# Kernel optimization log

Hardware: AMD Instinct MI355X
Metric: run time of the kernel (lower is better)

The kernel has to match this reference:

```python
import jax, jax.numpy as jnp
import numpy as np

B, L, D, N = 2, 2048, 1024, 16
DT_MIN, DT_MAX = 1e-3, 1e-1


def setup_inputs() -> dict:
    key = jax.random.key(0)
    ks = jax.random.split(key, 8)
    u = jax.random.normal(ks[0], (B, L, D), dtype=jnp.float32)
    # torch.nn.Linear weights are (out_features, in_features)
    W_dt = jax.random.normal(ks[1], (D, D), dtype=jnp.float32) * 0.02
    b_dt = jnp.zeros((D,), dtype=jnp.float32)
    W_B = jax.random.normal(ks[2], (D * N, D), dtype=jnp.float32) * 0.02
    b_B = jnp.zeros((D * N,), dtype=jnp.float32)
    W_C = jax.random.normal(ks[3], (D * N, D), dtype=jnp.float32) * 0.02
    b_C = jnp.zeros((D * N,), dtype=jnp.float32)
    # log_A init: log(1..N) broadcast over channels (HiPPO-ish diagonal)
    log_A = jnp.broadcast_to(jnp.log(jnp.arange(1, N + 1, dtype=jnp.float32)), (D, N))
    D_skip = jnp.ones((D,), dtype=jnp.float32)
    lo, hi = float(np.log(DT_MIN)), float(np.log(DT_MAX))
    dt_bias = jax.random.uniform(ks[4], (D,), dtype=jnp.float32) * (hi - lo) + lo
    return {"u": u, "log_A": log_A, "D_skip": D_skip, "dt_bias": dt_bias,
            "W_dt": W_dt, "b_dt": b_dt, "W_B": W_B, "b_B": b_B,
            "W_C": W_C, "b_C": b_C}


def reference(u, log_A, D_skip, dt_bias, W_dt, b_dt, W_B, b_B, W_C, b_C):
    b, l, d = u.shape
    n = log_A.shape[1]
    A = -jnp.exp(log_A)                                   # (d, n), A < 0
    # token-dependent parameters, computed for all timesteps at once
    dt = jax.nn.softplus(u @ W_dt.T + b_dt + dt_bias)     # (b, l, d)
    Bt = (u @ W_B.T + b_B).reshape(b, l, d, n)            # (b, l, d, n)
    Ct = (u @ W_C.T + b_C).reshape(b, l, d, n)            # (b, l, d, n)
    # exact ZOH discretisation
    A_bar = jnp.exp(dt[..., None] * A)                    # (b, l, d, n)
    B_bar = (A_bar - 1.0) / A * Bt                        # (b, l, d, n)
    x_in = B_bar * u[..., None]                           # (b, l, d, n)
    # recurrent scan over time
    def step(h, inp):
        a_t, x_t, c_t = inp                               # each (b, d, n)
        h = a_t * h + x_t
        y_t = jnp.sum(c_t * h, axis=-1)                   # (b, d)
        return h, y_t
    h0 = jnp.zeros((b, d, n), dtype=u.dtype)
    xs = (jnp.moveaxis(A_bar, 1, 0), jnp.moveaxis(x_in, 1, 0), jnp.moveaxis(Ct, 1, 0))
    _, ys = jax.lax.scan(step, h0, xs)                    # ys: (l, b, d)
    y = jnp.moveaxis(ys, 0, 1) + D_skip * u               # (b, l, d)
    return y
```

## Files before the change

### kernel.cpp

```cpp
#include <hip/hip_runtime.h>
#include <hip/hip_bf16.h>
#include <stdint.h>

constexpr int Bb = 2;
constexpr int Ll = 2048;
constexpr int Dd = 1024;
constexpr int Nn = 16;
constexpr int NB = Dd * Nn;
constexpr int SL = 64;
constexpr int NCH = Bb * Dd;
constexpr int KCAT = 3 * Dd;

typedef __bf16 bf16_t;
typedef __bf16 bf16x8 __attribute__((ext_vector_type(8)));
typedef __bf16 bf16x4 __attribute__((ext_vector_type(4)));
typedef float f32x4 __attribute__((ext_vector_type(4)));

__device__ inline void gld_lds16(const void* g, void* l) {
    __builtin_amdgcn_global_load_lds(
        (const __attribute__((address_space(1))) unsigned int*)g,
        (__attribute__((address_space(3))) unsigned int*)l, 16, 0, 0);
}

__global__ __launch_bounds__(256) void cvt_bf16(const float* __restrict__ s,
                                                bf16_t* __restrict__ d, int n4) {
    int i = blockIdx.x * 256 + threadIdx.x;
    const int stride = gridDim.x * 256;
    const float4* s4 = (const float4*)s;
    bf16x4* d4 = (bf16x4*)d;
    for (; i < n4; i += stride) {
        float4 v = s4[i];
        bf16x4 o = {(bf16_t)v.x, (bf16_t)v.y, (bf16_t)v.z, (bf16_t)v.w};
        d4[i] = o;
    }
}

__global__ __launch_bounds__(256) void build_ucat(const float* __restrict__ u,
                                                  bf16_t* __restrict__ ucat) {
    const int i = blockIdx.x * 256 + threadIdx.x;
    const int row = i >> 8;
    const int c = (i & 255) << 2;
    float4 v = ((const float4*)u)[i];
    bf16x4 hi = {(bf16_t)v.x, (bf16_t)v.y, (bf16_t)v.z, (bf16_t)v.w};
    bf16x4 lo = {(bf16_t)(v.x - (float)hi.x), (bf16_t)(v.y - (float)hi.y),
                 (bf16_t)(v.z - (float)hi.z), (bf16_t)(v.w - (float)hi.w)};
    bf16_t* r = ucat + (size_t)row * KCAT;
    *(bf16x4*)(r + c) = hi;
    *(bf16x4*)(r + Dd + c) = lo;
    *(bf16x4*)(r + 2 * Dd + c) = hi;
}

__global__ __launch_bounds__(256) void build_wcat(const float* __restrict__ w,
                                                  bf16_t* __restrict__ wcat) {
    const int i = blockIdx.x * 256 + threadIdx.x;
    const int row = i >> 8;
    const int c = (i & 255) << 2;
    float4 v = ((const float4*)w)[i];
    bf16x4 hi = {(bf16_t)v.x, (bf16_t)v.y, (bf16_t)v.z, (bf16_t)v.w};
    bf16x4 lo = {(bf16_t)(v.x - (float)hi.x), (bf16_t)(v.y - (float)hi.y),
                 (bf16_t)(v.z - (float)hi.z), (bf16_t)(v.w - (float)hi.w)};
    bf16_t* r = wcat + (size_t)row * KCAT;
    *(bf16x4*)(r + c) = hi;
    *(bf16x4*)(r + Dd + c) = hi;
    *(bf16x4*)(r + 2 * Dd + c) = lo;
}

template <int EP, typename OutT>
__global__ __launch_bounds__(256) void gemm_mfma(
    const bf16_t* __restrict__ Abase, int CL, int l0, int K,
    const bf16_t* __restrict__ W, const float* __restrict__ b1,
    const float* __restrict__ b2, OutT* __restrict__ C, int N)
{
    __shared__ bf16_t As[128 * 32];
    __shared__ bf16_t Bs[128 * 32];

    const int tid = threadIdx.x;
    const int bn = blockIdx.x * 128;
    const int rglob = blockIdx.y * 128;
    const int batch = rglob / CL;
    const int rin = rglob % CL;
    const bf16_t* Ap = Abase + ((size_t)batch * Ll + l0 + rin) * K;
    const bf16_t* Wp = W + (size_t)bn * K;
    OutT* Cp = C + (size_t)rglob * N;

    const int sr = tid >> 2;
    const int sc = (tid & 3) << 3;
    char* ldsA = (char*)As + tid * 16;
    char* ldsB = (char*)Bs + tid * 16;

    const int lane = tid & 63;
    const int wid = tid >> 6;
    const int wm = (wid & 1) << 6;
    const int wn = (wid >> 1) << 6;
    const int lr = lane & 15;
    const int lq = lane >> 4;

    f32x4 acc[4][4] = {};

    for (int k0 = 0; k0 < K; k0 += 32) {
        __syncthreads();
        gld_lds16(Ap + (size_t)sr * K + k0 + sc, ldsA);
        gld_lds16(Ap + (size_t)(sr + 64) * K + k0 + sc, ldsA + 4096);
        gld_lds16(Wp + (size_t)sr * K + k0 + sc, ldsB);
        gld_lds16(Wp + (size_t)(sr + 64) * K + k0 + sc, ldsB + 4096);
        __syncthreads();

        bf16x8 af[4], bfr[4];
#pragma unroll
        for (int mi = 0; mi < 4; ++mi)
            af[mi] = *(const bf16x8*)&As[(wm + mi * 16 + lr) * 32 + lq * 8];
#pragma unroll
        for (int ni = 0; ni < 4; ++ni)
            bfr[ni] = *(const bf16x8*)&Bs[(wn + ni * 16 + lr) * 32 + lq * 8];
#pragma unroll
        for (int mi = 0; mi < 4; ++mi)
#pragma unroll
            for (int ni = 0; ni < 4; ++ni)
                acc[mi][ni] = __builtin_amdgcn_mfma_f32_16x16x32_bf16(
                    af[mi], bfr[ni], acc[mi][ni], 0, 0, 0);
    }

#pragma unroll
    for (int ni = 0; ni < 4; ++ni) {
        const int col = bn + wn + ni * 16 + lr;
        const float bc = b1[col] + (EP == 1 ? b2[col] : 0.f);
#pragma unroll
        for (int mi = 0; mi < 4; ++mi)
#pragma unroll
            for (int i = 0; i < 4; ++i) {
                float v = acc[mi][ni][i] + bc;
                if (EP == 1) v = (v > 20.f) ? v : log1pf(__expf(v));
                Cp[(size_t)(wm + mi * 16 + lq * 4 + i) * N + col] = (OutT)v;
            }
    }
}

__global__ __launch_bounds__(256) void scan_seg_local(
    const float* __restrict__ u, const float* __restrict__ dt,
    const bf16_t* __restrict__ Bt_c, const float* __restrict__ log_A,
    float* __restrict__ pseg, float* __restrict__ hseg, int CL, int l0)
{
    const int tid = threadIdx.x;
    const int g = tid >> 4, n = tid & 15;
    const int gid = blockIdx.x * 16 + g;
    const int ch = gid & (NCH - 1);
    const int s = gid >> 11;
    const int b = ch >> 10, d = ch & (Dd - 1);

    const float A = -__expf(log_A[d * Nn + n]);
    const float rA = 1.f / A;

    size_t idx_bn = (size_t)(b * CL + s * SL) * NB + d * Nn + n;
    size_t idx_u = ((size_t)b * Ll + l0 + s * SL) * Dd + d;

    float p = 1.f, h = 0.f;
    for (int l = 0; l < SL; ++l) {
        const float dtv = dt[idx_u];
        const float uv = u[idx_u];
        const float bv = (float)Bt_c[idx_bn];
        const float a = __expf(dtv * A);
        p *= a;
        h = a * h + (a - 1.f) * rA * bv * uv;
        idx_bn += NB; idx_u += Dd;
    }
    const size_t o = ((size_t)s * NCH + ch) * Nn + n;
    pseg[o] = p;
    hseg[o] = h;
}

__global__ __launch_bounds__(256) void scan_combine(
    const float* __restrict__ pseg, const float* __restrict__ hseg,
    float* __restrict__ hin_arr, float* __restrict__ h_state,
    int NSEG, int l0)
{
    const int t = blockIdx.x * 256 + threadIdx.x;
    float hin = (l0 == 0) ? 0.f : h_state[t];
    for (int s = 0; s < NSEG; ++s) {
        const size_t o = (size_t)s * (NCH * Nn) + t;
        hin_arr[o] = hin;
        hin = pseg[o] * hin + hseg[o];
    }
    h_state[t] = hin;
}

__global__ __launch_bounds__(256) void scan_seg_final(
    const float* __restrict__ u, const float* __restrict__ dt,
    const bf16_t* __restrict__ Bt_c, const bf16_t* __restrict__ Ct_c,
    const float* __restrict__ log_A, const float* __restrict__ D_skip,
    const float* __restrict__ hin_arr, float* __restrict__ y, int CL, int l0)
{
    const int tid = threadIdx.x;
    const int g = tid >> 4, n = tid & 15;
    const int gid = blockIdx.x * 16 + g;
    const int ch = gid & (NCH - 1);
    const int s = gid >> 11;
    const int b = ch >> 10, d = ch & (Dd - 1);

    const float A = -__expf(log_A[d * Nn + n]);
    const float rA = 1.f / A;
    const float Dsk = D_skip[d];

    size_t idx_bn = (size_t)(b * CL + s * SL) * NB + d * Nn + n;
    size_t idx_u = ((size_t)b * Ll + l0 + s * SL) * Dd + d;

    float h = hin_arr[((size_t)s * NCH + ch) * Nn + n];
    for (int l = 0; l < SL; ++l) {
        const float dtv = dt[idx_u];
        const float uv = u[idx_u];
        const float bv = (float)Bt_c[idx_bn];
        const float cv = (float)Ct_c[idx_bn];
        const float a = __expf(dtv * A);
        h = a * h + (a - 1.f) * rA * bv * uv;
        float p = cv * h;
        p += __shfl_xor(p, 1);
        p += __shfl_xor(p, 2);
        p += __shfl_xor(p, 4);
        p += __shfl_xor(p, 8);
        if (n == 0) y[idx_u] = p + Dsk * uv;
        idx_bn += NB; idx_u += Dd;
    }
}

static inline size_t al256(size_t x) { return (x + 255) & ~(size_t)255; }

extern "C" void kernel_launch(void* const* d_in, const int* in_sizes, int n_in,
                              void* d_out, int out_size, void* d_ws, size_t ws_size,
                              hipStream_t stream) {
    const float* u       = (const float*)d_in[0];
    const float* log_A   = (const float*)d_in[1];
    const float* D_skip  = (const float*)d_in[2];
    const float* dt_bias = (const float*)d_in[3];
    const float* W_dt    = (const float*)d_in[4];
    const float* b_dt    = (const float*)d_in[5];
    const float* W_B     = (const float*)d_in[6];
    const float* b_B     = (const float*)d_in[7];
    const float* W_C     = (const float*)d_in[8];
    const float* b_C     = (const float*)d_in[9];
    float* y = (float*)d_out;

    const size_t sz_ubf  = al256((size_t)Bb * Ll * Dd * 2);
    const size_t sz_w    = al256((size_t)NB * Dd * 2);
    const size_t sz_h    = al256((size_t)NCH * Nn * 4);
    const size_t sz_dtf  = al256((size_t)Bb * Ll * Dd * 4);
    const size_t sz_ucat = al256((size_t)Bb * Ll * KCAT * 2);
    const size_t sz_wcat = al256((size_t)Dd * KCAT * 2);

    int CL = 128;
    const int cands[5] = {2048, 1024, 512, 256, 128};
    for (int i = 0; i < 5; ++i) {
        const int c = cands[i];
        const int nseg = c / SL;
        const size_t seg = 3 * al256((size_t)nseg * NCH * Nn * 4);
        const size_t chunk = 2 * al256((size_t)2 * c * NB * 2);
        const size_t ovl = sz_ucat + sz_wcat;
        const size_t need = sz_ubf + 2 * sz_w + sz_h + sz_dtf + seg +
                            (chunk > ovl ? chunk : ovl);
        if (need <= ws_size) { CL = c; break; }
    }
    const int NSEG = CL / SL;

    char* p = (char*)d_ws;
    bf16_t* u_bf   = (bf16_t*)p; p += sz_ubf;
    bf16_t* wB_bf  = (bf16_t*)p; p += sz_w;
    bf16_t* wC_bf  = (bf16_t*)p; p += sz_w;
    float* h_state = (float*)p; p += sz_h;
    float* dt_full = (float*)p; p += sz_dtf;
    const size_t sz_seg1 = al256((size_t)NSEG * NCH * Nn * 4);
    float* pseg    = (float*)p; p += sz_seg1;
    float* hseg    = (float*)p; p += sz_seg1;
    float* hin_arr = (float*)p; p += sz_seg1;
    char* chunk0 = p;
    bf16_t* Bt_c = (bf16_t*)chunk0;
    bf16_t* Ct_c = (bf16_t*)(chunk0 + al256((size_t)2 * CL * NB * 2));
    bf16_t* u_cat = (bf16_t*)chunk0;
    bf16_t* w_cat = (bf16_t*)(chunk0 + sz_ucat);

    cvt_bf16<<<2048, 256, 0, stream>>>(u, u_bf, Bb * Ll * Dd / 4);
    cvt_bf16<<<2048, 256, 0, stream>>>(W_B, wB_bf, NB * Dd / 4);
    cvt_bf16<<<2048, 256, 0, stream>>>(W_C, wC_bf, NB * Dd / 4);
    build_ucat<<<Bb * Ll * Dd / 4 / 256, 256, 0, stream>>>(u, u_cat);
    build_wcat<<<Dd * Dd / 4 / 256, 256, 0, stream>>>(W_dt, w_cat);

    gemm_mfma<1, float><<<dim3(Dd / 128, Bb * Ll / 128), 256, 0, stream>>>(
        u_cat, Ll, 0, KCAT, w_cat, b_dt, dt_bias, dt_full, Dd);

    for (int l0 = 0; l0 < Ll; l0 += CL) {
        gemm_mfma<0, bf16_t><<<dim3(NB / 128, 2 * CL / 128), 256, 0, stream>>>(
            u_bf, CL, l0, Dd, wB_bf, b_B, nullptr, Bt_c, NB);
        gemm_mfma<0, bf16_t><<<dim3(NB / 128, 2 * CL / 128), 256, 0, stream>>>(
            u_bf, CL, l0, Dd, wC_bf, b_C, nullptr, Ct_c, NB);
        scan_seg_local<<<dim3(128 * NSEG), 256, 0, stream>>>(
            u, dt_full, Bt_c, log_A, pseg, hseg, CL, l0);
        scan_combine<<<dim3(128), 256, 0, stream>>>(
            pseg, hseg, hin_arr, h_state, NSEG, l0);
        scan_seg_final<<<dim3(128 * NSEG), 256, 0, stream>>>(
            u, dt_full, Bt_c, Ct_c, log_A, D_skip, hin_arr, y, CL, l0);
    }
}
```

Before: 800.0 us.

## Fuse B/C projection GEMMs, merge conversions, retile dt GEMM to 64x64

Concatenates W_B and W_C into one bf16 weight, so a single GEMM produces an interleaved B/C buffer that both scan kernels read. The u bf16 conversion is folded into build_ucat and the two weight conversions share one launch, removing kernel launches and one pass over u. The dt GEMM moves to a dedicated 64x64-tile kernel, giving more blocks to fill the GPU. The interleaved layout doubles the row stride of the B/C reads in the scan.

```diff
diff --git a/kernel.cpp b/kernel.cpp
--- a/kernel.cpp
+++ b/kernel.cpp
@@ -7,6 +7,7 @@
 constexpr int Dd = 1024;
 constexpr int Nn = 16;
 constexpr int NB = Dd * Nn;
+constexpr int NB2 = 2 * NB;
 constexpr int SL = 64;
 constexpr int NCH = Bb * Dd;
 constexpr int KCAT = 3 * Dd;
@@ -22,21 +23,9 @@
         (__attribute__((address_space(3))) unsigned int*)l, 16, 0, 0);
 }
 
-__global__ __launch_bounds__(256) void cvt_bf16(const float* __restrict__ s,
-                                                bf16_t* __restrict__ d, int n4) {
-    int i = blockIdx.x * 256 + threadIdx.x;
-    const int stride = gridDim.x * 256;
-    const float4* s4 = (const float4*)s;
-    bf16x4* d4 = (bf16x4*)d;
-    for (; i < n4; i += stride) {
-        float4 v = s4[i];
-        bf16x4 o = {(bf16_t)v.x, (bf16_t)v.y, (bf16_t)v.z, (bf16_t)v.w};
-        d4[i] = o;
-    }
-}
-
 __global__ __launch_bounds__(256) void build_ucat(const float* __restrict__ u,
-                                                  bf16_t* __restrict__ ucat) {
+                                                  bf16_t* __restrict__ ucat,
+                                                  bf16_t* __restrict__ ubf) {
     const int i = blockIdx.x * 256 + threadIdx.x;
     const int row = i >> 8;
     const int c = (i & 255) << 2;
@@ -48,6 +37,7 @@
     *(bf16x4*)(r + c) = hi;
     *(bf16x4*)(r + Dd + c) = lo;
     *(bf16x4*)(r + 2 * Dd + c) = hi;
+    *(bf16x4*)(ubf + (size_t)i * 4) = hi;
 }
 
 __global__ __launch_bounds__(256) void build_wcat(const float* __restrict__ w,
@@ -65,12 +55,26 @@
     *(bf16x4*)(r + 2 * Dd + c) = lo;
 }
 
-template <int EP, typename OutT>
-__global__ __launch_bounds__(256) void gemm_mfma(
-    const bf16_t* __restrict__ Abase, int CL, int l0, int K,
-    const bf16_t* __restrict__ W, const float* __restrict__ b1,
-    const float* __restrict__ b2, OutT* __restrict__ C, int N)
-{
+__global__ __launch_bounds__(256) void cvt_wbc(const float* __restrict__ wB,
+                                               const float* __restrict__ wC,
+                                               bf16_t* __restrict__ d) {
+    const int half = NB * Dd / 4;
+    int i = blockIdx.x * 256 + threadIdx.x;
+    const int stride = gridDim.x * 256;
+    for (; i < 2 * half; i += stride) {
+        float4 v = (i < half) ? ((const float4*)wB)[i]
+                              : ((const float4*)wC)[i - half];
+        bf16x4 o = {(bf16_t)v.x, (bf16_t)v.y, (bf16_t)v.z, (bf16_t)v.w};
+        *(bf16x4*)(d + (size_t)i * 4) = o;
+    }
+}
+
+__global__ __launch_bounds__(256) void gemm_bc(
+    const bf16_t* __restrict__ Abase, int CL, int l0,
+    const bf16_t* __restrict__ W, const float* __restrict__ bB,
+    const float* __restrict__ bC, bf16_t* __restrict__ C)
+{
+    constexpr int K = Dd;
     __shared__ bf16_t As[128 * 32];
     __shared__ bf16_t Bs[128 * 32];
 
@@ -81,7 +85,7 @@
     const int rin = rglob % CL;
     const bf16_t* Ap = Abase + ((size_t)batch * Ll + l0 + rin) * K;
     const bf16_t* Wp = W + (size_t)bn * K;
-    OutT* Cp = C + (size_t)rglob * N;
+    bf16_t* Cp = C + (size_t)rglob * NB2;
 
     const int sr = tid >> 2;
     const int sc = (tid & 3) << 3;
@@ -123,21 +127,74 @@
 #pragma unroll
     for (int ni = 0; ni < 4; ++ni) {
         const int col = bn + wn + ni * 16 + lr;
-        const float bc = b1[col] + (EP == 1 ? b2[col] : 0.f);
+        const float bc = (col < NB) ? bB[col] : bC[col - NB];
 #pragma unroll
         for (int mi = 0; mi < 4; ++mi)
 #pragma unroll
-            for (int i = 0; i < 4; ++i) {
-                float v = acc[mi][ni][i] + bc;
-                if (EP == 1) v = (v > 20.f) ? v : log1pf(__expf(v));
-                Cp[(size_t)(wm + mi * 16 + lq * 4 + i) * N + col] = (OutT)v;
-            }
+            for (int i = 0; i < 4; ++i)
+                Cp[(size_t)(wm + mi * 16 + lq * 4 + i) * NB2 + col] =
+                    (bf16_t)(acc[mi][ni][i] + bc);
+    }
+}
+
+__global__ __launch_bounds__(256) void gemm_dt64(
+    const bf16_t* __restrict__ ucat, const bf16_t* __restrict__ wcat,
+    const float* __restrict__ b1, const float* __restrict__ b2,
+    float* __restrict__ dt)
+{
+    constexpr int K = KCAT;
+    __shared__ bf16_t As[64 * 32];
+    __shared__ bf16_t Bs[64 * 32];
+
+    const int tid = threadIdx.x;
+    const int bn = blockIdx.x * 64;
+    const int bm = blockIdx.y * 64;
+    const bf16_t* Ap = ucat + (size_t)bm * K;
+    const bf16_t* Wp = wcat + (size_t)bn * K;
+
+    const int sr = tid >> 2;
+    const int sc = (tid & 3) << 3;
+    char* ldsA = (char*)As + tid * 16;
+    char* ldsB = (char*)Bs + tid * 16;
+
+    const int lane = tid & 63;
+    const int w = tid >> 6;
+    const int lr = lane & 15;
+    const int lq = lane >> 4;
+
+    f32x4 acc[4] = {};
+
+    for (int k0 = 0; k0 < K; k0 += 32) {
+        __syncthreads();
+        gld_lds16(Ap + (size_t)sr * K + k0 + sc, ldsA);
+        gld_lds16(Wp + (size_t)sr * K + k0 + sc, ldsB);
+        __syncthreads();
+
+        const bf16x8 af = *(const bf16x8*)&As[(w * 16 + lr) * 32 + lq * 8];
+#pragma unroll
+        for (int ni = 0; ni < 4; ++ni) {
+            const bf16x8 bf = *(const bf16x8*)&Bs[(ni * 16 + lr) * 32 + lq * 8];
+            acc[ni] = __builtin_amdgcn_mfma_f32_16x16x32_bf16(af, bf, acc[ni], 0, 0, 0);
+        }
+    }
+
+#pragma unroll
+    for (int ni = 0; ni < 4; ++ni) {
+        const int col = bn + ni * 16 + lr;
+        const float bc = b1[col] + b2[col];
+#pragma unroll
+        for (int i = 0; i < 4; ++i) {
+            const int row = bm + w * 16 + lq * 4 + i;
+            float v = acc[ni][i] + bc;
+            v = (v > 20.f) ? v : log1pf(__expf(v));
+            dt[(size_t)row * Dd + col] = v;
+        }
     }
 }
 
 __global__ __launch_bounds__(256) void scan_seg_local(
     const float* __restrict__ u, const float* __restrict__ dt,
-    const bf16_t* __restrict__ Bt_c, const float* __restrict__ log_A,
+    const bf16_t* __restrict__ BC, const float* __restrict__ log_A,
     float* __restrict__ pseg, float* __restrict__ hseg, int CL, int l0)
 {
     const int tid = threadIdx.x;
@@ -150,18 +207,18 @@
     const float A = -__expf(log_A[d * Nn + n]);
     const float rA = 1.f / A;
 
-    size_t idx_bn = (size_t)(b * CL + s * SL) * NB + d * Nn + n;
+    size_t idx_bn = (size_t)(b * CL + s * SL) * NB2 + d * Nn + n;
     size_t idx_u = ((size_t)b * Ll + l0 + s * SL) * Dd + d;
 
     float p = 1.f, h = 0.f;
     for (int l = 0; l < SL; ++l) {
         const float dtv = dt[idx_u];
         const float uv = u[idx_u];
-        const float bv = (float)Bt_c[idx_bn];
+        const float bv = (float)BC[idx_bn];
         const float a = __expf(dtv * A);
         p *= a;
         h = a * h + (a - 1.f) * rA * bv * uv;
-        idx_bn += NB; idx_u += Dd;
+        idx_bn += NB2; idx_u += Dd;
     }
     const size_t o = ((size_t)s * NCH + ch) * Nn + n;
     pseg[o] = p;
@@ -185,9 +242,9 @@
 
 __global__ __launch_bounds__(256) void scan_seg_final(
     const float* __restrict__ u, const float* __restrict__ dt,
-    const bf16_t* __restrict__ Bt_c, const bf16_t* __restrict__ Ct_c,
-    const float* __restrict__ log_A, const float* __restrict__ D_skip,
-    const float* __restrict__ hin_arr, float* __restrict__ y, int CL, int l0)
+    const bf16_t* __restrict__ BC, const float* __restrict__ log_A,
+    const float* __restrict__ D_skip, const float* __restrict__ hin_arr,
+    float* __restrict__ y, int CL, int l0)
 {
     const int tid = threadIdx.x;
     const int g = tid >> 4, n = tid & 15;
@@ -200,15 +257,15 @@
     const float rA = 1.f / A;
     const float Dsk = D_skip[d];
 
-    size_t idx_bn = (size_t)(b * CL + s * SL) * NB + d * Nn + n;
+    size_t idx_bn = (size_t)(b * CL + s * SL) * NB2 + d * Nn + n;
     size_t idx_u = ((size_t)b * Ll + l0 + s * SL) * Dd + d;
 
     float h = hin_arr[((size_t)s * NCH + ch) * Nn + n];
     for (int l = 0; l < SL; ++l) {
         const float dtv = dt[idx_u];
         const float uv = u[idx_u];
-        const float bv = (float)Bt_c[idx_bn];
-        const float cv = (float)Ct_c[idx_bn];
+        const float bv = (float)BC[idx_bn];
+        const float cv = (float)BC[idx_bn + NB];
         const float a = __expf(dtv * A);
         h = a * h + (a - 1.f) * rA * bv * uv;
         float p = cv * h;
@@ -217,7 +274,7 @@
         p += __shfl_xor(p, 4);
         p += __shfl_xor(p, 8);
         if (n == 0) y[idx_u] = p + Dsk * uv;
-        idx_bn += NB; idx_u += Dd;
+        idx_bn += NB2; idx_u += Dd;
     }
 }
 
@@ -239,7 +296,7 @@
     float* y = (float*)d_out;
 
     const size_t sz_ubf  = al256((size_t)Bb * Ll * Dd * 2);
-    const size_t sz_w    = al256((size_t)NB * Dd * 2);
+    const size_t sz_wbc  = al256((size_t)NB2 * Dd * 2);
     const size_t sz_h    = al256((size_t)NCH * Nn * 4);
     const size_t sz_dtf  = al256((size_t)Bb * Ll * Dd * 4);
     const size_t sz_ucat = al256((size_t)Bb * Ll * KCAT * 2);
@@ -251,9 +308,9 @@
         const int c = cands[i];
         const int nseg = c / SL;
         const size_t seg = 3 * al256((size_t)nseg * NCH * Nn * 4);
-        const size_t chunk = 2 * al256((size_t)2 * c * NB * 2);
+        const size_t chunk = al256((size_t)2 * c * NB2 * 2);
         const size_t ovl = sz_ucat + sz_wcat;
-        const size_t need = sz_ubf + 2 * sz_w + sz_h + sz_dtf + seg +
+        const size_t need = sz_ubf + sz_wbc + sz_h + sz_dtf + seg +
                             (chunk > ovl ? chunk : ovl);
         if (need <= ws_size) { CL = c; break; }
     }
@@ -261,8 +318,7 @@
 
     char* p = (char*)d_ws;
     bf16_t* u_bf   = (bf16_t*)p; p += sz_ubf;
-    bf16_t* wB_bf  = (bf16_t*)p; p += sz_w;
-    bf16_t* wC_bf  = (bf16_t*)p; p += sz_w;
+    bf16_t* wBC    = (bf16_t*)p; p += sz_wbc;
     float* h_state = (float*)p; p += sz_h;
     float* dt_full = (float*)p; p += sz_dtf;
     const size_t sz_seg1 = al256((size_t)NSEG * NCH * Nn * 4);
@@ -270,30 +326,25 @@
     float* hseg    = (float*)p; p += sz_seg1;
     float* hin_arr = (float*)p; p += sz_seg1;
     char* chunk0 = p;
-    bf16_t* Bt_c = (bf16_t*)chunk0;
-    bf16_t* Ct_c = (bf16_t*)(chunk0 + al256((size_t)2 * CL * NB * 2));
+    bf16_t* BC_c  = (bf16_t*)chunk0;
     bf16_t* u_cat = (bf16_t*)chunk0;
     bf16_t* w_cat = (bf16_t*)(chunk0 + sz_ucat);
 
-    cvt_bf16<<<2048, 256, 0, stream>>>(u, u_bf, Bb * Ll * Dd / 4);
-    cvt_bf16<<<2048, 256, 0, stream>>>(W_B, wB_bf, NB * Dd / 4);
-    cvt_bf16<<<2048, 256, 0, stream>>>(W_C, wC_bf, NB * Dd / 4);
-    build_ucat<<<Bb * Ll * Dd / 4 / 256, 256, 0, stream>>>(u, u_cat);
+    build_ucat<<<Bb * Ll * Dd / 4 / 256, 256, 0, stream>>>(u, u_cat, u_bf);
     build_wcat<<<Dd * Dd / 4 / 256, 256, 0, stream>>>(W_dt, w_cat);
-
-    gemm_mfma<1, float><<<dim3(Dd / 128, Bb * Ll / 128), 256, 0, stream>>>(
-        u_cat, Ll, 0, KCAT, w_cat, b_dt, dt_bias, dt_full, Dd);
+    cvt_wbc<<<2048, 256, 0, stream>>>(W_B, W_C, wBC);
+
+    gemm_dt64<<<dim3(Dd / 64, Bb * Ll / 64), 256, 0, stream>>>(
+        u_cat, w_cat, b_dt, dt_bias, dt_full);
 
     for (int l0 = 0; l0 < Ll; l0 += CL) {
-        gemm_mfma<0, bf16_t><<<dim3(NB / 128, 2 * CL / 128), 256, 0, stream>>>(
-            u_bf, CL, l0, Dd, wB_bf, b_B, nullptr, Bt_c, NB);
-        gemm_mfma<0, bf16_t><<<dim3(NB / 128, 2 * CL / 128), 256, 0, stream>>>(
-            u_bf, CL, l0, Dd, wC_bf, b_C, nullptr, Ct_c, NB);
+        gemm_bc<<<dim3(NB2 / 128, 2 * CL / 128), 256, 0, stream>>>(
+            u_bf, CL, l0, wBC, b_B, b_C, BC_c);
         scan_seg_local<<<dim3(128 * NSEG), 256, 0, stream>>>(
-            u, dt_full, Bt_c, log_A, pseg, hseg, CL, l0);
+            u, dt_full, BC_c, log_A, pseg, hseg, CL, l0);
         scan_combine<<<dim3(128), 256, 0, stream>>>(
             pseg, hseg, hin_arr, h_state, NSEG, l0);
         scan_seg_final<<<dim3(128 * NSEG), 256, 0, stream>>>(
-            u, dt_full, Bt_c, Ct_c, log_A, D_skip, hin_arr, y, CL, l0);
-    }
-}
+            u, dt_full, BC_c, log_A, D_skip, hin_arr, y, CL, l0);
+    }
+}
```

Measured after the change: 853.6 us. 6.7% more time.
